# Kernel optimization log

Measured on AMD Instinct MI355X. Metric: run time of the kernel, lower is better.

Reference implementation:

```python
import jax, jax.numpy as jnp
import numpy as np

KERNEL_SIZE = 4  # W


def setup_inputs() -> dict:
    key = jax.random.key(0)
    k1, k2, k3, k4 = jax.random.split(key, 4)
    B, T, D, H, W = 2, 4096, 2048, 2048, KERNEL_SIZE
    x = jax.random.normal(k1, (B, T, D), dtype=jnp.float32)
    # torch nn.Linear weight layout: [out_features, in_features]
    w1 = jax.random.normal(k2, (H, D), dtype=jnp.float32) * 0.02
    w2_w = jax.random.normal(k3, (D * W, H), dtype=jnp.float32) * 0.02
    w2_b = jax.random.normal(k4, (D * W,), dtype=jnp.float32) * 0.02
    return {"x": x, "w1": w1, "w2_w": w2_w, "w2_b": w2_b}


def reference(x, w1, w2_w, w2_b):
    # x: [B, T, D]
    B, T, D = x.shape
    W = KERNEL_SIZE
    # kernel generator MLP: Linear(D->H, no bias) -> silu -> Linear(H->D*W, bias)
    h = jax.nn.silu(jnp.einsum('btd,hd->bth', x, w1))
    flat_kernels = jnp.einsum('bth,kh->btk', h, w2_w) + w2_b
    # rearrange 'b t (d w) -> b t d w' (d major, w minor)
    kernels = flat_kernels.reshape(B, T, D, W)
    # causal windows: pad W-1 on the left of time, gather W shifted views
    x_pad = jnp.pad(x, ((0, 0), (W - 1, 0), (0, 0)))
    windows = jnp.stack([x_pad[:, w:w + T, :] for w in range(W)], axis=-1)  # [B,T,D,W]
    out = jnp.sum(windows * kernels, axis=-1)  # per-token dynamic depthwise causal conv
    return jax.nn.silu(out)  # self.activation == 'silu'
```

## Files before the change

kernel.cpp:

```cpp
#include <hip/hip_runtime.h>
#include <hip/hip_bf16.h>
#include <math.h>

#define B_DIM 2
#define T_DIM 4096
#define D_DIM 2048
#define H_DIM 2048
#define W_K   4
#define M_DIM (B_DIM * T_DIM)
#define N2_DIM (D_DIM * W_K)

typedef __bf16 bf16x8 __attribute__((ext_vector_type(8)));
typedef float  f32x4  __attribute__((ext_vector_type(4)));

#define BM 256
#define BN 256
#define BKT 64
#define XW_STRIDE 68

__device__ __forceinline__ unsigned short f2bf(float f) {
    unsigned int u = __float_as_uint(f);
    unsigned int r = (u + 0x7FFFu + ((u >> 16) & 1u)) >> 16;
    return (unsigned short)r;
}

__device__ __forceinline__ float silu_f(float v) {
    return v / (1.0f + __expf(-v));
}

__global__ void cvt_f32_to_bf16(const float* __restrict__ in,
                                unsigned short* __restrict__ out, int n4) {
    int i = blockIdx.x * blockDim.x + threadIdx.x;
    if (i >= n4) return;
    float4 v = reinterpret_cast<const float4*>(in)[i];
    ushort4 o;
    o.x = f2bf(v.x); o.y = f2bf(v.y); o.z = f2bf(v.z); o.w = f2bf(v.w);
    reinterpret_cast<ushort4*>(out)[i] = o;
}

__device__ __forceinline__ bf16x8 lds_frag(const unsigned short* buf, int r, int kb) {
    int lin = r * 128 + (kb ^ ((r & 7) << 4));
    return *reinterpret_cast<const bf16x8*>(reinterpret_cast<const char*>(buf) + lin);
}

#define BARRIER()    __builtin_amdgcn_s_barrier()
#define WAIT_VM(N)   asm volatile("s_waitcnt vmcnt(" #N ")" ::: "memory")

#define STAGE64(basePtr, ko, dstUshort, chunk) \
    __builtin_amdgcn_global_load_lds( \
        (const __attribute__((address_space(1))) void*)((basePtr) + soff + (size_t)(chunk) * 64 * K + (ko)), \
        (__attribute__((address_space(3))) void*)(reinterpret_cast<char*>(dstUshort) + ((chunk) << 13) + (wave << 10)), \
        16, 0, 0)

#define MG_MFMA(mg, AF) \
    _Pragma("unroll") for (int kk = 0; kk < 2; ++kk) \
    _Pragma("unroll") for (int mrel = 0; mrel < 2; ++mrel) \
    _Pragma("unroll") for (int nf = 0; nf < 4; ++nf) \
        acc[(mg)*2 + mrel][nf] = __builtin_amdgcn_mfma_f32_16x16x32_bf16( \
            AF[mrel][kk], bfrag[nf][kk], acc[(mg)*2 + mrel][nf], 0, 0, 0)

#define READ_B(tB) \
    _Pragma("unroll") for (int nf = 0; nf < 4; ++nf) \
    _Pragma("unroll") for (int kk = 0; kk < 2; ++kk) \
        bfrag[nf][kk] = lds_frag(tB, wc*64 + nf*16 + ln15, kk*64 + kb16)

#define READ_A(AF, tA, mg) \
    _Pragma("unroll") for (int mrel = 0; mrel < 2; ++mrel) \
    _Pragma("unroll") for (int kk = 0; kk < 2; ++kk) \
        AF[mrel][kk] = lds_frag(tA, wr*128 + (mg)*32 + mrel*16 + ln15, kk*64 + kb16)

#define KTILE_R(bi, jj, SA2, SB, VMN) do { \
    const unsigned short* tA = smem + (bi) * 16384; \
    const unsigned short* tB = smem + 32768 + (bi) * 16384; \
    unsigned short* oA = smem + ((bi) ^ 1) * 16384; \
    unsigned short* cA = smem + (bi) * 16384; \
    unsigned short* cB = smem + 32768 + (bi) * 16384; \
    READ_B(tB); \
    READ_A(af0, tA, 0); \
    if (SA2) { const int ko = ((jj) + 1) << 6; \
        STAGE64(baseA, ko, oA, 1); STAGE64(baseA, ko, oA, 3); } \
    READ_A(af1, tA, 1); \
    __builtin_amdgcn_s_setprio(1); MG_MFMA(0, af0); __builtin_amdgcn_s_setprio(0); \
    __builtin_amdgcn_s_setprio(1); MG_MFMA(1, af1); __builtin_amdgcn_s_setprio(0); \
    BARRIER(); \
    READ_A(af0, tA, 2); \
    if (SB) { const int ko = ((jj) + 2) << 6; \
        STAGE64(baseB, ko, cB, 0); STAGE64(baseB, ko, cB, 1); \
        STAGE64(baseA, ko, cA, 0); STAGE64(baseA, ko, cA, 2); } \
    READ_A(af1, tA, 3); \
    __builtin_amdgcn_s_setprio(1); MG_MFMA(2, af0); __builtin_amdgcn_s_setprio(0); \
    if (SB) { const int ko = ((jj) + 2) << 6; \
        STAGE64(baseB, ko, cB, 2); STAGE64(baseB, ko, cB, 3); } \
    __builtin_amdgcn_s_setprio(1); MG_MFMA(3, af1); __builtin_amdgcn_s_setprio(0); \
    WAIT_VM(VMN); \
    BARRIER(); \
} while (0)

template <int EPI>
__global__ __launch_bounds__(512, 2)
void gemm8p(const unsigned short* __restrict__ A,
            const unsigned short* __restrict__ Bm,
            int M, int N, int K,
            unsigned short* __restrict__ Hout,
            const float* __restrict__ bias,
            const float* __restrict__ Xf,
            float* __restrict__ Out) {
    __shared__ __align__(16) unsigned short smem[65536];

    const int tid  = threadIdx.x;
    const int wave = tid >> 6, lane = tid & 63;
    const int wr = wave >> 2, wc = wave & 3;
    const int ln15 = lane & 15;
    const int kb16 = (lane >> 4) * 16;

    const int GX = gridDim.x, GY = gridDim.y;
    const int bid = blockIdx.y * GX + blockIdx.x;
    const int xcd = bid & 7;
    const int idx = bid >> 3;
    const int W_ = GX >> 2;
    const int rr = idx / W_, cc = idx % W_;
    const int by = (xcd >> 2) * (GY >> 1) + rr;
    const int bx = (xcd & 3) * W_ + cc;
    const int m0 = by * BM, n0 = bx * BN;

    const int nk = K >> 6;

    const int srow = (wave << 3) + (lane >> 3);
    const int scol = (((lane & 7) ^ ((lane >> 3) & 7)) << 3);
    const size_t soff = (size_t)srow * K + scol;
    const unsigned short* baseA = A + (size_t)m0 * K;
    const unsigned short* baseB = Bm + (size_t)n0 * K;

    f32x4 acc[8][4];
#pragma unroll
    for (int i = 0; i < 8; ++i)
#pragma unroll
        for (int j = 0; j < 4; ++j) acc[i][j] = (f32x4)0.0f;

    bf16x8 bfrag[4][2], af0[2][2], af1[2][2];

    {
        unsigned short* dA0 = smem;
        unsigned short* dB0 = smem + 32768;
        unsigned short* dA1 = smem + 16384;
        unsigned short* dB1 = smem + 49152;
        STAGE64(baseB, 0, dB0, 0); STAGE64(baseB, 0, dB0, 1);
        STAGE64(baseB, 0, dB0, 2); STAGE64(baseB, 0, dB0, 3);
        STAGE64(baseA, 0, dA0, 0); STAGE64(baseA, 0, dA0, 1);
        STAGE64(baseA, 0, dA0, 2); STAGE64(baseA, 0, dA0, 3);
        STAGE64(baseB, BKT, dB1, 0); STAGE64(baseB, BKT, dB1, 1);
        STAGE64(baseA, BKT, dA1, 0); STAGE64(baseA, BKT, dA1, 2);
        STAGE64(baseB, BKT, dB1, 2); STAGE64(baseB, BKT, dB1, 3);
    }
    WAIT_VM(6);
    BARRIER();

    for (int it = 0; it < (nk >> 1) - 1; ++it) {
        const int j = it << 1;
        KTILE_R(0, j,     1, 1, 6);
        KTILE_R(1, j + 1, 1, 1, 6);
    }
    KTILE_R(0, nk - 2, 1, 0, 0);
    KTILE_R(1, nk - 1, 0, 0, 0);

    if (EPI == 0) {
#pragma unroll
        for (int mf = 0; mf < 8; ++mf) {
            int rowb = m0 + wr * 128 + mf * 16 + (lane >> 4) * 4;
#pragma unroll
            for (int nf = 0; nf < 4; ++nf) {
                int col = n0 + wc * 64 + nf * 16 + ln15;
#pragma unroll
                for (int r2 = 0; r2 < 4; ++r2) {
                    Hout[(size_t)(rowb + r2) * N + col] = f2bf(silu_f(acc[mf][nf][r2]));
                }
            }
        }
    } else {
        const int t0 = m0 & (T_DIM - 1);
        const int bidx = m0 >> 12;
        const int dbase = n0 >> 2;
        float* Xw = reinterpret_cast<float*>(smem);
        for (int idx2 = tid; idx2 < 259 * 16; idx2 += 512) {
            int rw = idx2 >> 4, q = (idx2 & 15) << 2;
            int ts = t0 - 3 + rw;
            float4 v = make_float4(0.f, 0.f, 0.f, 0.f);
            if (ts >= 0)
                v = *reinterpret_cast<const float4*>(
                    &Xf[((size_t)bidx * T_DIM + ts) * D_DIM + dbase + q]);
            float* p = &Xw[rw * XW_STRIDE + q];
            p[0] = v.x; p[1] = v.y; p[2] = v.z; p[3] = v.w;
        }
        __syncthreads();

        const int dl = wc * 16 + (ln15 >> 2);
        const int w = lane & 3;
#pragma unroll
        for (int mf = 0; mf < 8; ++mf) {
            int lrow0 = wr * 128 + mf * 16 + (lane >> 4) * 4;
#pragma unroll
            for (int nf = 0; nf < 4; ++nf) {
                int col = n0 + wc * 64 + nf * 16 + ln15;
                int d = col >> 2;
                float bv = bias[col];
#pragma unroll
                for (int r2 = 0; r2 < 4; ++r2) {
                    int lrow = lrow0 + r2;
                    float v = acc[mf][nf][r2] + bv;
                    float xv = Xw[(lrow + w) * XW_STRIDE + dl + nf * 4];
                    float p = v * xv;
                    p += __shfl_xor(p, 1);
                    p += __shfl_xor(p, 2);
                    if ((lane & 3) == 0) {
                        Out[((size_t)bidx * T_DIM + (t0 + lrow)) * D_DIM + d] = silu_f(p);
                    }
                }
            }
        }
    }
}

extern "C" void kernel_launch(void* const* d_in, const int* in_sizes, int n_in,
                              void* d_out, int out_size, void* d_ws, size_t ws_size,
                              hipStream_t stream) {
    const float* x    = (const float*)d_in[0];
    const float* w1   = (const float*)d_in[1];
    const float* w2w  = (const float*)d_in[2];
    const float* w2b  = (const float*)d_in[3];
    float* out = (float*)d_out;

    unsigned short* ws0 = (unsigned short*)d_ws;
    unsigned short* ws1 = ws0 + (size_t)M_DIM * D_DIM;
    unsigned short* ws2 = ws1 + (size_t)H_DIM * D_DIM;

    const int CT = 256;
    {
        int n4 = (M_DIM * D_DIM) / 4;
        cvt_f32_to_bf16<<<(n4 + CT - 1) / CT, CT, 0, stream>>>(x, ws0, n4);
    }
    {
        int n4 = (H_DIM * D_DIM) / 4;
        cvt_f32_to_bf16<<<(n4 + CT - 1) / CT, CT, 0, stream>>>(w1, ws1, n4);
    }
    gemm8p<0><<<dim3(H_DIM / BN, M_DIM / BM), 512, 0, stream>>>(
        ws0, ws1, M_DIM, H_DIM, D_DIM, ws2, nullptr, nullptr, nullptr);
    {
        int n4 = (N2_DIM * H_DIM) / 4;
        cvt_f32_to_bf16<<<(n4 + CT - 1) / CT, CT, 0, stream>>>(w2w, ws0, n4);
    }
    gemm8p<1><<<dim3(N2_DIM / BN, M_DIM / BM), 512, 0, stream>>>(
        ws2, ws0, M_DIM, N2_DIM, H_DIM, nullptr, w2b, x, out);
}
```

Measured before the change: 401.8 us.

## Remap B fragment columns so each lane owns contiguous outputs in epilogues

```diff
diff --git a/kernel.cpp b/kernel.cpp
--- a/kernel.cpp
+++ b/kernel.cpp
@@ -39,7 +39,8 @@
 }
 
 __device__ __forceinline__ bf16x8 lds_frag(const unsigned short* buf, int r, int kb) {
-    int lin = r * 128 + (kb ^ ((r & 7) << 4));
+    int sx = (((r & 7) ^ ((r >> 3) & 7)) << 4);
+    int lin = r * 128 + (kb ^ sx);
     return *reinterpret_cast<const bf16x8*>(reinterpret_cast<const char*>(buf) + lin);
 }
 
@@ -62,7 +63,7 @@
 #define READ_B(tB) \
     _Pragma("unroll") for (int nf = 0; nf < 4; ++nf) \
     _Pragma("unroll") for (int kk = 0; kk < 2; ++kk) \
-        bfrag[nf][kk] = lds_frag(tB, wc*64 + nf*16 + ln15, kk*64 + kb16)
+        bfrag[nf][kk] = lds_frag(tB, wc*64 + ln15*4 + nf, kk*64 + kb16)
 
 #define READ_A(AF, tA, mg) \
     _Pragma("unroll") for (int mrel = 0; mrel < 2; ++mrel) \
@@ -126,7 +127,7 @@
     const int nk = K >> 6;
 
     const int srow = (wave << 3) + (lane >> 3);
-    const int scol = (((lane & 7) ^ ((lane >> 3) & 7)) << 3);
+    const int scol = (((lane & 7) ^ (lane >> 3) ^ wave) << 3);
     const size_t soff = (size_t)srow * K + scol;
     const unsigned short* baseA = A + (size_t)m0 * K;
     const unsigned short* baseB = Bm + (size_t)n0 * K;
@@ -164,16 +165,18 @@
     KTILE_R(1, nk - 1, 0, 0, 0);
 
     if (EPI == 0) {
+        const size_t colbase = n0 + wc * 64 + ln15 * 4;
 #pragma unroll
         for (int mf = 0; mf < 8; ++mf) {
             int rowb = m0 + wr * 128 + mf * 16 + (lane >> 4) * 4;
 #pragma unroll
-            for (int nf = 0; nf < 4; ++nf) {
-                int col = n0 + wc * 64 + nf * 16 + ln15;
-#pragma unroll
-                for (int r2 = 0; r2 < 4; ++r2) {
-                    Hout[(size_t)(rowb + r2) * N + col] = f2bf(silu_f(acc[mf][nf][r2]));
-                }
+            for (int r2 = 0; r2 < 4; ++r2) {
+                ushort4 h4;
+                h4.x = f2bf(silu_f(acc[mf][0][r2]));
+                h4.y = f2bf(silu_f(acc[mf][1][r2]));
+                h4.z = f2bf(silu_f(acc[mf][2][r2]));
+                h4.w = f2bf(silu_f(acc[mf][3][r2]));
+                *reinterpret_cast<ushort4*>(&Hout[(size_t)(rowb + r2) * N + colbase]) = h4;
             }
         }
     } else {
@@ -193,28 +196,24 @@
         }
         __syncthreads();
 
-        const int dl = wc * 16 + (ln15 >> 2);
-        const int w = lane & 3;
+        const int dloc = wc * 16 + ln15;
+        const float4 bias4 = *reinterpret_cast<const float4*>(
+            &bias[n0 + wc * 64 + ln15 * 4]);
 #pragma unroll
         for (int mf = 0; mf < 8; ++mf) {
             int lrow0 = wr * 128 + mf * 16 + (lane >> 4) * 4;
-#pragma unroll
-            for (int nf = 0; nf < 4; ++nf) {
-                int col = n0 + wc * 64 + nf * 16 + ln15;
-                int d = col >> 2;
-                float bv = bias[col];
-#pragma unroll
-                for (int r2 = 0; r2 < 4; ++r2) {
-                    int lrow = lrow0 + r2;
-                    float v = acc[mf][nf][r2] + bv;
-                    float xv = Xw[(lrow + w) * XW_STRIDE + dl + nf * 4];
-                    float p = v * xv;
-                    p += __shfl_xor(p, 1);
-                    p += __shfl_xor(p, 2);
-                    if ((lane & 3) == 0) {
-                        Out[((size_t)bidx * T_DIM + (t0 + lrow)) * D_DIM + d] = silu_f(p);
-                    }
-                }
+            float xr[7];
+#pragma unroll
+            for (int q = 0; q < 7; ++q)
+                xr[q] = Xw[(lrow0 + q) * XW_STRIDE + dloc];
+#pragma unroll
+            for (int r2 = 0; r2 < 4; ++r2) {
+                float v = (acc[mf][0][r2] + bias4.x) * xr[r2 + 0];
+                v      += (acc[mf][1][r2] + bias4.y) * xr[r2 + 1];
+                v      += (acc[mf][2][r2] + bias4.z) * xr[r2 + 2];
+                v      += (acc[mf][3][r2] + bias4.w) * xr[r2 + 3];
+                int lrow = lrow0 + r2;
+                Out[((size_t)bidx * T_DIM + (t0 + lrow)) * D_DIM + dbase + dloc] = silu_f(v);
             }
         }
     }
```

New measurement: 369.5 us. 8.0% less time.
